# Optimization experiments

Hardware: AMD Instinct MI355X
Metric: run time of the kernel (lower is better)

## Reference

```python
import jax, jax.numpy as jnp
import numpy as np

K_MAX, K_MIN = 12.0, 1.0
TEMP = 1.0
STE_ALPHA = 12.0
EPS = 1e-8

DIM, HID, KHID, WHID = 512, 2048, 128, 128
B, N = 8, 1024


def setup_inputs() -> dict:
    key = jax.random.key(0)
    ks = jax.random.split(key, 13)
    def lin(k, fan_in, shape):
        bound = 1.0 / np.sqrt(fan_in)
        return jax.random.uniform(k, shape, jnp.float32, -bound, bound)
    return {
        "x": jax.random.normal(ks[0], (B, N, DIM), jnp.float32),
        "fc1_w": lin(ks[1], DIM, (HID, DIM)),
        "fc1_b": lin(ks[2], DIM, (HID,)),
        "fc2_w": lin(ks[3], HID, (DIM, HID)),
        "fc2_b": lin(ks[4], HID, (DIM,)),
        "k1_w": lin(ks[5], DIM, (KHID, DIM)),
        "k1_b": lin(ks[6], DIM, (KHID,)),
        "k2_w": lin(ks[7], KHID, (3, KHID)),
        "k2_b": lin(ks[8], KHID, (3,)),
        "w1_w": lin(ks[9], DIM, (WHID, DIM)),
        "w1_b": lin(ks[10], DIM, (WHID,)),
        "w2_w": lin(ks[11], WHID, (3, WHID)),
        "w2_b": lin(ks[12], WHID, (3,)),
    }


def adaptive_knn_aggregate(h, k_cont):
    # h: (B,N,C), k_cont: (B,) continuous k in [k_min, k_max]
    sim = jnp.einsum("bnc,bmc->bnm", h, h) / TEMP          # (B,N,N)
    order = jnp.argsort(-sim, axis=-1)                      # descending
    rank = jnp.argsort(order, axis=-1).astype(h.dtype)      # rank 0 = most similar
    # soft top-k gate (STE-style sigmoid around k_cont)
    gate = jax.nn.sigmoid(STE_ALPHA * (k_cont[:, None, None] - (rank + 0.5)))
    attn = jax.nn.softmax(sim, axis=-1) * gate
    attn = attn / (attn.sum(axis=-1, keepdims=True) + EPS)
    return jnp.einsum("bnm,bmc->bnc", attn, h)


def reference(x, fc1_w, fc1_b, fc2_w, fc2_b, k1_w, k1_b, k2_w, k2_b,
              w1_w, w1_b, w2_w, w2_b):
    pooled = x.mean(axis=1)                                 # (B,C)
    # adaptive k values net
    kh = jax.nn.relu(pooled @ k1_w.T + k1_b)
    ratio = jax.nn.sigmoid(kh @ k2_w.T + k2_b)              # (B,3)
    k_cont = K_MIN + ratio * (K_MAX - K_MIN)
    # adaptive branch weights net
    wh = jax.nn.relu(pooled @ w1_w.T + w1_b)
    w = jax.nn.softmax(wh @ w2_w.T + w2_b, axis=-1)         # (B,3)
    # MLP (dropout p=0 -> identity)
    h = jax.nn.relu(x @ fc1_w.T + fc1_b)
    h = h @ fc2_w.T + fc2_b                                 # (B,N,C)
    # three KNN aggregation branches blended by w
    y = sum(adaptive_knn_aggregate(h, k_cont[:, i]) * w[:, i, None, None]
            for i in range(3))
    return y
```

## Files before the change

### kernel.cpp

```cpp
#include <hip/hip_runtime.h>
#include <math.h>

#define DIM_ 512
#define HID_ 2048
#define B_ 8
#define N_ 1024
#define ROWS_ 8192
#define TOPK 16

typedef __attribute__((ext_vector_type(8))) short short8;
typedef __attribute__((ext_vector_type(16))) float float16v;

__device__ __forceinline__ float sigm(float x) { return 1.f / (1.f + __expf(-x)); }

__device__ __forceinline__ short f2bf(float f) {
    unsigned u = __float_as_uint(f);
    u += 0x7FFF + ((u >> 16) & 1);
    return (short)(u >> 16);
}

__device__ __forceinline__ float bf2f(unsigned short s) {
    return __uint_as_float((unsigned)s << 16);
}

__device__ __forceinline__ unsigned f2ord(float f) {
    unsigned u = __float_as_uint(f);
    return (u & 0x80000000u) ? ~u : (u | 0x80000000u);
}

__device__ __forceinline__ void gload16(const short* g, short* l) {
    __builtin_amdgcn_global_load_lds(
        (const __attribute__((address_space(1))) void*)g,
        (__attribute__((address_space(3))) void*)l, 16, 0, 0);
}

__global__ __launch_bounds__(512)
void prep_kernel(const float* __restrict__ x, float* __restrict__ part, short* __restrict__ xb,
                 const float* __restrict__ w1, const float* __restrict__ w2,
                 short* __restrict__ o1, short* __restrict__ o2) {
    const int bx = blockIdx.x;
    if (bx < 256) {
        const int b = bx >> 5, chunk = bx & 31;
        const int c = threadIdx.x;
        const long long base = ((long long)b * N_ + chunk * 32) * DIM_ + c;
        const float* xp = x + base;
        short* xo = xb + base;
        float s = 0.f;
        for (int n = 0; n < 32; ++n) {
            const float v = xp[(long long)n * DIM_];
            s += v;
            xo[(long long)n * DIM_] = f2bf(v);
        }
        part[(long long)bx * DIM_ + c] = s;
    } else {
        const int n4 = HID_ * DIM_ / 4;
        int i = (bx - 256) * 2048 + threadIdx.x;
#pragma unroll
        for (int t = 0; t < 4; ++t, i += 512) {
            const float* in = (i < n4) ? w1 : w2;
            short* out = (i < n4) ? o1 : o2;
            const int j = (i < n4) ? i : (i - n4);
            const float4 v = *(const float4*)(in + (long long)j * 4);
            short4 o;
            o.x = f2bf(v.x); o.y = f2bf(v.y); o.z = f2bf(v.z); o.w = f2bf(v.w);
            *(short4*)(out + (long long)j * 4) = o;
        }
    }
}

__global__ __launch_bounds__(512)
void pool_heads_kernel(const float* __restrict__ part,
                       const float* __restrict__ k1w, const float* __restrict__ k1b,
                       const float* __restrict__ k2w, const float* __restrict__ k2b,
                       const float* __restrict__ w1w, const float* __restrict__ w1b,
                       const float* __restrict__ w2w, const float* __restrict__ w2b,
                       float* __restrict__ kcont, float* __restrict__ wbr) {
    const int b = blockIdx.x;
    const int t = threadIdx.x;
    __shared__ float sp[DIM_];
    __shared__ float kh[128], wh[128];
    __shared__ float wraw[4];
    float s = 0.f;
    for (int g = 0; g < 32; ++g) s += part[((long long)b * 32 + g) * DIM_ + t];
    sp[t] = s * (1.f / 1024.f);
    __syncthreads();
    if (t < 128) {
        float ak = k1b[t], aw = w1b[t];
        for (int k = 0; k < DIM_; ++k) {
            const float pv = sp[k];
            ak = fmaf(pv, k1w[t * DIM_ + k], ak);
            aw = fmaf(pv, w1w[t * DIM_ + k], aw);
        }
        kh[t] = fmaxf(ak, 0.f);
        wh[t] = fmaxf(aw, 0.f);
    }
    __syncthreads();
    if (t < 3) {
        float rk = k2b[t], rw = w2b[t];
        for (int k = 0; k < 128; ++k) {
            rk = fmaf(kh[k], k2w[t * 128 + k], rk);
            rw = fmaf(wh[k], w2w[t * 128 + k], rw);
        }
        kcont[b * 3 + t] = 1.f + 11.f * sigm(rk);
        wraw[t] = rw;
    }
    __syncthreads();
    if (t == 0) {
        const float m = fmaxf(wraw[0], fmaxf(wraw[1], wraw[2]));
        const float e0 = __expf(wraw[0] - m), e1 = __expf(wraw[1] - m), e2 = __expf(wraw[2] - m);
        const float inv = 1.f / (e0 + e1 + e2);
        wbr[b * 3 + 0] = e0 * inv;
        wbr[b * 3 + 1] = e1 * inv;
        wbr[b * 3 + 2] = e2 * inv;
    }
}

template<int OUTMODE>
__global__ __launch_bounds__(256)
void gemm_mfma(const short* __restrict__ A, const short* __restrict__ Bm,
               const float* __restrict__ bias,
               float* __restrict__ outF, short* __restrict__ outB,
               int M, int N, int K, int lda, int ldb,
               long long sA, long long sB, long long sC) {
    const int bz = blockIdx.z;
    A  += (long long)bz * sA;
    Bm += (long long)bz * sB;

    __shared__ short As[128 * 64];
    __shared__ short Bs[128 * 64];

    const int tid = threadIdx.x;
    const int lane = tid & 63;
    const int wv = tid >> 6;
    const int m0 = blockIdx.y * 128;
    const int n0 = blockIdx.x * 128;

    const int lrow = lane >> 3;
    const int cg = (lane & 7) ^ lrow;

    const int ml = (wv & 1) * 64;
    const int nl = (wv >> 1) * 64;
    const int fr = lane & 31;
    const int kh = lane >> 5;

    float16v acc[2][2];
#pragma unroll
    for (int i = 0; i < 2; ++i)
#pragma unroll
        for (int j = 0; j < 2; ++j)
#pragma unroll
            for (int r = 0; r < 16; ++r) acc[i][j][r] = 0.f;

    for (int k0 = 0; k0 < K; k0 += 64) {
        __syncthreads();
#pragma unroll
        for (int i = 0; i < 4; ++i) {
            const int rloc = wv * 32 + i * 8 + lrow;
            gload16(A + (long long)(m0 + rloc) * lda + (k0 + cg * 8),
                    &As[(wv * 32 + i * 8) * 64]);
            gload16(Bm + (long long)(n0 + rloc) * ldb + (k0 + cg * 8),
                    &Bs[(wv * 32 + i * 8) * 64]);
        }
        __syncthreads();
#pragma unroll
        for (int c = 0; c < 4; ++c) {
            const int ch = c * 2 + kh;
            short8 af[2], bfr[2];
#pragma unroll
            for (int i = 0; i < 2; ++i) {
                const int m = ml + i * 32 + fr;
                af[i] = *(const short8*)&As[m * 64 + ((ch ^ (m & 7)) * 8)];
                const int n = nl + i * 32 + fr;
                bfr[i] = *(const short8*)&Bs[n * 64 + ((ch ^ (n & 7)) * 8)];
            }
#pragma unroll
            for (int i = 0; i < 2; ++i)
#pragma unroll
                for (int j = 0; j < 2; ++j)
                    acc[i][j] = __builtin_amdgcn_mfma_f32_32x32x16_bf16(
                        af[i], bfr[j], acc[i][j], 0, 0, 0);
        }
    }

    const long long outOfs = (long long)bz * sC;
#pragma unroll
    for (int i = 0; i < 2; ++i) {
#pragma unroll
        for (int j = 0; j < 2; ++j) {
            const int ng = n0 + nl + j * 32 + fr;
            float bv = 0.f;
            if (OUTMODE != 2) bv = bias[ng];
#pragma unroll
            for (int r = 0; r < 16; ++r) {
                const int mg = m0 + ml + i * 32 + (r & 3) + 8 * (r >> 2) + 4 * kh;
                float v = acc[i][j][r] + bv;
                if (OUTMODE == 0) v = fmaxf(v, 0.f);
                const long long idx = outOfs + (long long)mg * N + ng;
                if (OUTMODE == 2) outF[idx] = v;
                else              outB[idx] = f2bf(v);
            }
        }
    }
}

__global__ __launch_bounds__(256)
void combine_kernel(const float* __restrict__ p0, const float* __restrict__ p1,
                    const float* __restrict__ bias, short* __restrict__ out) {
    const int i = blockIdx.x * 256 + threadIdx.x;
    const long long o = (long long)i * 4;
    const float4 a = *(const float4*)(p0 + o);
    const float4 b = *(const float4*)(p1 + o);
    const int col = (int)(o & (DIM_ - 1));
    const float4 bs = *(const float4*)(bias + col);
    short4 r;
    r.x = f2bf(a.x + b.x + bs.x);
    r.y = f2bf(a.y + b.y + bs.y);
    r.z = f2bf(a.z + b.z + bs.z);
    r.w = f2bf(a.w + b.w + bs.w);
    *(short4*)(out + o) = r;
}

__global__ __launch_bounds__(256)
void topk_agg_kernel(const float* __restrict__ sim,
                     const float* __restrict__ kcont, const float* __restrict__ wbr,
                     const unsigned short* __restrict__ h, float* __restrict__ y) {
    const int wv = threadIdx.x >> 6;
    const int lane = threadIdx.x & 63;
    const int ll = lane & 15;
    const int row = blockIdx.x * 4 + wv;
    const int b = row >> 10;
    const float* srow = sim + (long long)row * N_;

    float f[16];
    const int base = lane * 16;
#pragma unroll
    for (int q = 0; q < 4; ++q) {
        const float4 v = *(const float4*)(srow + base + q * 4);
        f[q * 4 + 0] = v.x; f[q * 4 + 1] = v.y; f[q * 4 + 2] = v.z; f[q * 4 + 3] = v.w;
    }

    float lmax = f[0];
#pragma unroll
    for (int j = 1; j < 16; ++j) lmax = fmaxf(lmax, f[j]);
#pragma unroll
    for (int d = 32; d > 0; d >>= 1) lmax = fmaxf(lmax, __shfl_xor(lmax, d));
    const float maxv = lmax;

    float lsum = 0.f;
#pragma unroll
    for (int j = 0; j < 16; ++j) lsum += __expf(f[j] - maxv);
#pragma unroll
    for (int d = 32; d > 0; d >>= 1) lsum += __shfl_xor(lsum, d);
    const float invden = 1.f / lsum;

    unsigned key[16];
#pragma unroll
    for (int j = 0; j < 16; ++j)
        key[j] = (f2ord(f[j]) & 0xFFFFFC00u) | (unsigned)(1023 - (base + j));

#pragma unroll
    for (int k = 2; k <= 16; k <<= 1) {
#pragma unroll
        for (int j = k >> 1; j > 0; j >>= 1) {
#pragma unroll
            for (int i = 0; i < 16; ++i) {
                const int l = i ^ j;
                if (l > i) {
                    const bool desc = ((i & k) == 0);
                    const unsigned a = key[i], bk = key[l];
                    const unsigned hi = (a > bk) ? a : bk;
                    const unsigned lo = (a > bk) ? bk : a;
                    key[i] = desc ? hi : lo;
                    key[l] = desc ? lo : hi;
                }
            }
        }
    }

#pragma unroll
    for (int d = 1; d < 64; d <<= 1) {
        unsigned other[16];
#pragma unroll
        for (int i = 0; i < 16; ++i)
            other[i] = __shfl_xor(key[15 - i], d);
#pragma unroll
        for (int i = 0; i < 16; ++i)
            key[i] = (key[i] > other[i]) ? key[i] : other[i];
#pragma unroll
        for (int j = 8; j > 0; j >>= 1) {
#pragma unroll
            for (int i = 0; i < 16; ++i) {
                if ((i & j) == 0) {
                    const unsigned a = key[i], bk = key[i | j];
                    key[i]     = (a > bk) ? a : bk;
                    key[i | j] = (a > bk) ? bk : a;
                }
            }
        }
    }

    unsigned k32 = key[0];
#pragma unroll
    for (int j = 1; j < 16; ++j) k32 = (ll == j) ? key[j] : k32;
    const int myidx = 1023 - (int)(k32 & 1023u);
    const float myval = srow[myidx];

    unsigned long long kx = ((unsigned long long)f2ord(myval) << 32)
                          | (unsigned)(1023 - myidx);
#pragma unroll
    for (int k = 2; k <= 16; k <<= 1) {
#pragma unroll
        for (int d = k >> 1; d > 0; d >>= 1) {
            const unsigned long long other = __shfl_xor(kx, d);
            const bool keepMax = (((ll & k) != 0) == ((ll & d) != 0));
            const bool mineBig = (kx > other);
            kx = (keepMax == mineBig) ? kx : other;
        }
    }
    const unsigned sord = (unsigned)(kx >> 32);
    const unsigned su = (sord & 0x80000000u) ? (sord & 0x7FFFFFFFu) : ~sord;
    const float sval = __uint_as_float(su);
    const int sidx = 1023 - (int)(kx & 1023u);

    const float kc0 = kcont[b * 3 + 0], kc1 = kcont[b * 3 + 1], kc2 = kcont[b * 3 + 2];
    const float w0 = wbr[b * 3 + 0], w1 = wbr[b * 3 + 1], w2 = wbr[b * 3 + 2];

    const float p = __expf(sval - maxv) * invden;
    const float rr = (float)ll + 0.5f;
    const float g0 = sigm(12.f * (kc0 - rr));
    const float g1 = sigm(12.f * (kc1 - rr));
    const float g2 = sigm(12.f * (kc2 - rr));
    float s0 = p * g0, s1 = p * g1, s2 = p * g2;
#pragma unroll
    for (int d = 1; d < 16; d <<= 1) {
        s0 += __shfl_xor(s0, d);
        s1 += __shfl_xor(s1, d);
        s2 += __shfl_xor(s2, d);
    }
    const float f0 = w0 / (s0 + 1e-8f);
    const float f1 = w1 / (s1 + 1e-8f);
    const float f2 = w2 / (s2 + 1e-8f);
    const float mycoef = p * (f0 * g0 + f1 * g1 + f2 * g2);

    const int gbase = lane & 48;
    const unsigned short* hbase = h + (long long)b * (N_ * DIM_) + lane * 8;
    float acc[8] = {0.f, 0.f, 0.f, 0.f, 0.f, 0.f, 0.f, 0.f};
#pragma unroll
    for (int r = 0; r < 16; ++r) {
        const float coef = __shfl(mycoef, gbase | r);
        const int idx = __shfl(sidx, gbase | r);
        const ushort4 h0 = *(const ushort4*)(hbase + (long long)idx * DIM_);
        const ushort4 h1 = *(const ushort4*)(hbase + (long long)idx * DIM_ + 4);
        acc[0] = fmaf(coef, bf2f(h0.x), acc[0]);
        acc[1] = fmaf(coef, bf2f(h0.y), acc[1]);
        acc[2] = fmaf(coef, bf2f(h0.z), acc[2]);
        acc[3] = fmaf(coef, bf2f(h0.w), acc[3]);
        acc[4] = fmaf(coef, bf2f(h1.x), acc[4]);
        acc[5] = fmaf(coef, bf2f(h1.y), acc[5]);
        acc[6] = fmaf(coef, bf2f(h1.z), acc[6]);
        acc[7] = fmaf(coef, bf2f(h1.w), acc[7]);
    }
    float* yp = y + (long long)row * DIM_ + lane * 8;
    *(float4*)(yp + 0) = make_float4(acc[0], acc[1], acc[2], acc[3]);
    *(float4*)(yp + 4) = make_float4(acc[4], acc[5], acc[6], acc[7]);
}

extern "C" void kernel_launch(void* const* d_in, const int* in_sizes, int n_in,
                              void* d_out, int out_size, void* d_ws, size_t ws_size,
                              hipStream_t stream) {
    const float* x     = (const float*)d_in[0];
    const float* fc1_w = (const float*)d_in[1];
    const float* fc1_b = (const float*)d_in[2];
    const float* fc2_w = (const float*)d_in[3];
    const float* fc2_b = (const float*)d_in[4];
    const float* k1_w  = (const float*)d_in[5];
    const float* k1_b  = (const float*)d_in[6];
    const float* k2_w  = (const float*)d_in[7];
    const float* k2_b  = (const float*)d_in[8];
    const float* w1_w  = (const float*)d_in[9];
    const float* w1_b  = (const float*)d_in[10];
    const float* w2_w  = (const float*)d_in[11];
    const float* w2_b  = (const float*)d_in[12];

    char* ws = (char*)d_ws;
    short* h1b    = (short*)(ws + 0);
    float* simbuf = (float*)(ws + 0);
    short* xb     = (short*)(ws + 33554432);
    float* part0  = (float*)(ws + 33554432);
    float* part1  = (float*)(ws + 50331648);
    short* hb     = (short*)(ws + 67108864);
    short* w1b    = (short*)(ws + 75497472);
    short* w2b    = (short*)(ws + 77594624);
    float* ppart  = (float*)(ws + 79691776);
    float* kcont  = (float*)(ws + 80216064);
    float* wbr    = (float*)(ws + 80216192);

    float* y = (float*)d_out;

    prep_kernel<<<dim3(512), dim3(512), 0, stream>>>(x, ppart, xb, fc1_w, fc2_w, w1b, w2b);
    pool_heads_kernel<<<dim3(B_), dim3(512), 0, stream>>>(ppart, k1_w, k1_b, k2_w, k2_b,
                                                          w1_w, w1_b, w2_w, w2_b, kcont, wbr);
    gemm_mfma<0><<<dim3(HID_ / 128, ROWS_ / 128, 1), dim3(256), 0, stream>>>(
        xb, w1b, fc1_b, nullptr, h1b, ROWS_, HID_, DIM_, DIM_, DIM_, 0, 0, 0);
    gemm_mfma<2><<<dim3(DIM_ / 128, ROWS_ / 128, 2), dim3(256), 0, stream>>>(
        h1b, w2b, nullptr, part0, nullptr, ROWS_, DIM_, HID_ / 2, HID_, HID_,
        (long long)(HID_ / 2), (long long)(HID_ / 2), (long long)ROWS_ * DIM_);
    combine_kernel<<<dim3(ROWS_ * DIM_ / 4 / 256), dim3(256), 0, stream>>>(part0, part1, fc2_b, hb);
    gemm_mfma<2><<<dim3(N_ / 128, N_ / 128, B_), dim3(256), 0, stream>>>(
        hb, hb, nullptr, simbuf, nullptr, N_, N_, DIM_, DIM_, DIM_,
        (long long)N_ * DIM_, (long long)N_ * DIM_, (long long)N_ * N_);
    topk_agg_kernel<<<dim3(ROWS_ / 4), dim3(256), 0, stream>>>(
        simbuf, kcont, wbr, (const unsigned short*)hb, y);
}
```

Baseline: 221.2 us.

## Replace split-K fc2 GEMM and combine pass with single 128x64-tile GEMM

```diff
diff --git a/kernel.cpp b/kernel.cpp
--- a/kernel.cpp
+++ b/kernel.cpp
@@ -115,39 +115,40 @@
     }
 }
 
-template<int OUTMODE>
+template<int OUTMODE, int BN>
 __global__ __launch_bounds__(256)
 void gemm_mfma(const short* __restrict__ A, const short* __restrict__ Bm,
                const float* __restrict__ bias,
                float* __restrict__ outF, short* __restrict__ outB,
                int M, int N, int K, int lda, int ldb,
                long long sA, long long sB, long long sC) {
+    constexpr int NJ = BN / 64;
     const int bz = blockIdx.z;
     A  += (long long)bz * sA;
     Bm += (long long)bz * sB;
 
     __shared__ short As[128 * 64];
-    __shared__ short Bs[128 * 64];
+    __shared__ short Bs[BN * 64];
 
     const int tid = threadIdx.x;
     const int lane = tid & 63;
     const int wv = tid >> 6;
     const int m0 = blockIdx.y * 128;
-    const int n0 = blockIdx.x * 128;
+    const int n0 = blockIdx.x * BN;
 
     const int lrow = lane >> 3;
     const int cg = (lane & 7) ^ lrow;
 
     const int ml = (wv & 1) * 64;
-    const int nl = (wv >> 1) * 64;
+    const int nl = (wv >> 1) * (BN / 2);
     const int fr = lane & 31;
-    const int kh = lane >> 5;
-
-    float16v acc[2][2];
+    const int khh = lane >> 5;
+
+    float16v acc[2][NJ];
 #pragma unroll
     for (int i = 0; i < 2; ++i)
 #pragma unroll
-        for (int j = 0; j < 2; ++j)
+        for (int j = 0; j < NJ; ++j)
 #pragma unroll
             for (int r = 0; r < 16; ++r) acc[i][j][r] = 0.f;
 
@@ -158,25 +159,32 @@
             const int rloc = wv * 32 + i * 8 + lrow;
             gload16(A + (long long)(m0 + rloc) * lda + (k0 + cg * 8),
                     &As[(wv * 32 + i * 8) * 64]);
+        }
+#pragma unroll
+        for (int i = 0; i < BN / 32; ++i) {
+            const int rloc = wv * (BN / 4) + i * 8 + lrow;
             gload16(Bm + (long long)(n0 + rloc) * ldb + (k0 + cg * 8),
-                    &Bs[(wv * 32 + i * 8) * 64]);
+                    &Bs[(wv * (BN / 4) + i * 8) * 64]);
         }
         __syncthreads();
 #pragma unroll
         for (int c = 0; c < 4; ++c) {
-            const int ch = c * 2 + kh;
-            short8 af[2], bfr[2];
+            const int ch = c * 2 + khh;
+            short8 af[2], bfr[NJ];
 #pragma unroll
             for (int i = 0; i < 2; ++i) {
                 const int m = ml + i * 32 + fr;
                 af[i] = *(const short8*)&As[m * 64 + ((ch ^ (m & 7)) * 8)];
-                const int n = nl + i * 32 + fr;
-                bfr[i] = *(const short8*)&Bs[n * 64 + ((ch ^ (n & 7)) * 8)];
             }
 #pragma unroll
+            for (int j = 0; j < NJ; ++j) {
+                const int n = nl + j * 32 + fr;
+                bfr[j] = *(const short8*)&Bs[n * 64 + ((ch ^ (n & 7)) * 8)];
+            }
+#pragma unroll
             for (int i = 0; i < 2; ++i)
 #pragma unroll
-                for (int j = 0; j < 2; ++j)
+                for (int j = 0; j < NJ; ++j)
                     acc[i][j] = __builtin_amdgcn_mfma_f32_32x32x16_bf16(
                         af[i], bfr[j], acc[i][j], 0, 0, 0);
         }
@@ -186,13 +194,13 @@
 #pragma unroll
     for (int i = 0; i < 2; ++i) {
 #pragma unroll
-        for (int j = 0; j < 2; ++j) {
+        for (int j = 0; j < NJ; ++j) {
             const int ng = n0 + nl + j * 32 + fr;
             float bv = 0.f;
             if (OUTMODE != 2) bv = bias[ng];
 #pragma unroll
             for (int r = 0; r < 16; ++r) {
-                const int mg = m0 + ml + i * 32 + (r & 3) + 8 * (r >> 2) + 4 * kh;
+                const int mg = m0 + ml + i * 32 + (r & 3) + 8 * (r >> 2) + 4 * khh;
                 float v = acc[i][j][r] + bv;
                 if (OUTMODE == 0) v = fmaxf(v, 0.f);
                 const long long idx = outOfs + (long long)mg * N + ng;
@@ -201,23 +209,6 @@
             }
         }
     }
-}
-
-__global__ __launch_bounds__(256)
-void combine_kernel(const float* __restrict__ p0, const float* __restrict__ p1,
-                    const float* __restrict__ bias, short* __restrict__ out) {
-    const int i = blockIdx.x * 256 + threadIdx.x;
-    const long long o = (long long)i * 4;
-    const float4 a = *(const float4*)(p0 + o);
-    const float4 b = *(const float4*)(p1 + o);
-    const int col = (int)(o & (DIM_ - 1));
-    const float4 bs = *(const float4*)(bias + col);
-    short4 r;
-    r.x = f2bf(a.x + b.x + bs.x);
-    r.y = f2bf(a.y + b.y + bs.y);
-    r.z = f2bf(a.z + b.z + bs.z);
-    r.w = f2bf(a.w + b.w + bs.w);
-    *(short4*)(out + o) = r;
 }
 
 __global__ __launch_bounds__(256)
@@ -386,8 +377,6 @@
     short* h1b    = (short*)(ws + 0);
     float* simbuf = (float*)(ws + 0);
     short* xb     = (short*)(ws + 33554432);
-    float* part0  = (float*)(ws + 33554432);
-    float* part1  = (float*)(ws + 50331648);
     short* hb     = (short*)(ws + 67108864);
     short* w1b    = (short*)(ws + 75497472);
     short* w2b    = (short*)(ws + 77594624);
@@ -400,13 +389,11 @@
     prep_kernel<<<dim3(512), dim3(512), 0, stream>>>(x, ppart, xb, fc1_w, fc2_w, w1b, w2b);
     pool_heads_kernel<<<dim3(B_), dim3(512), 0, stream>>>(ppart, k1_w, k1_b, k2_w, k2_b,
                                                           w1_w, w1_b, w2_w, w2_b, kcont, wbr);
-    gemm_mfma<0><<<dim3(HID_ / 128, ROWS_ / 128, 1), dim3(256), 0, stream>>>(
+    gemm_mfma<0, 128><<<dim3(HID_ / 128, ROWS_ / 128, 1), dim3(256), 0, stream>>>(
         xb, w1b, fc1_b, nullptr, h1b, ROWS_, HID_, DIM_, DIM_, DIM_, 0, 0, 0);
-    gemm_mfma<2><<<dim3(DIM_ / 128, ROWS_ / 128, 2), dim3(256), 0, stream>>>(
-        h1b, w2b, nullptr, part0, nullptr, ROWS_, DIM_, HID_ / 2, HID_, HID_,
-        (long long)(HID_ / 2), (long long)(HID_ / 2), (long long)ROWS_ * DIM_);
-    combine_kernel<<<dim3(ROWS_ * DIM_ / 4 / 256), dim3(256), 0, stream>>>(part0, part1, fc2_b, hb);
-    gemm_mfma<2><<<dim3(N_ / 128, N_ / 128, B_), dim3(256), 0, stream>>>(
+    gemm_mfma<1, 64><<<dim3(DIM_ / 64, ROWS_ / 128, 1), dim3(256), 0, stream>>>(
+        h1b, w2b, fc2_b, nullptr, hb, ROWS_, DIM_, HID_, HID_, HID_, 0, 0, 0);
+    gemm_mfma<2, 128><<<dim3(N_ / 128, N_ / 128, B_), dim3(256), 0, stream>>>(
         hb, hb, nullptr, simbuf, nullptr, N_, N_, DIM_, DIM_, DIM_,
         (long long)N_ * DIM_, (long long)N_ * DIM_, (long long)N_ * N_);
     topk_agg_kernel<<<dim3(ROWS_ / 4), dim3(256), 0, stream>>>(
```

Measured after the change: 229.5 us. 1.04x slower.
